# Kernel tuning notes

Hardware: AMD Instinct MI355X
Metric: run time of the kernel (lower is better)

## Reference

```python
import jax, jax.numpy as jnp
import numpy as np

N_X = 32640   # total xlmr subword tokens (64 seqs x 510 tokens)
N_S = 16320   # total stanza word tokens (2 subwords per word)
E = 65280     # dependency edges (bidirectional, avg degree ~4)
D = 768
GCN_DIM = 256
GCN_NUM = 2
POS_DIM = 4
N_UPOS = 17
N_LABEL = 5


def setup_inputs() -> dict:
    key = jax.random.key(0)
    ks = jax.random.split(key, 8)
    x = jax.random.normal(ks[0], (N_X, D), dtype=jnp.float32)
    # mapStanza2Xlmr as segment ids: xlmr token j belongs to stanza word j//2
    seg = jnp.arange(N_X, dtype=jnp.int32) // 2
    edge_index = jax.random.randint(ks[1], (2, E), 0, N_S, dtype=jnp.int32)
    upos_ids = jax.random.randint(ks[2], (N_S,), 0, N_UPOS, dtype=jnp.int32)
    Wc = jax.random.normal(ks[3], (D, GCN_DIM), dtype=jnp.float32) * 0.02
    bc = jnp.zeros((GCN_DIM,), dtype=jnp.float32)
    gcn_W = jax.random.normal(ks[4], (GCN_NUM, GCN_DIM, GCN_DIM), dtype=jnp.float32) * 0.05
    gcn_b = jnp.zeros((GCN_NUM, GCN_DIM), dtype=jnp.float32)
    upos_table = jax.random.normal(ks[5], (N_UPOS, POS_DIM), dtype=jnp.float32)
    Wcls = jax.random.normal(ks[6], (D + GCN_DIM + POS_DIM, N_LABEL), dtype=jnp.float32) * 0.02
    bcls = jnp.zeros((N_LABEL,), dtype=jnp.float32)
    return {"x": x, "seg": seg, "edge_index": edge_index, "upos_ids": upos_ids,
            "Wc": Wc, "bc": bc, "gcn_W": gcn_W, "gcn_b": gcn_b,
            "upos_table": upos_table, "Wcls": Wcls, "bcls": bcls}


def _gcn_conv(h, srcs, dsts, W, b, n):
    # PyG GCNConv: h' = D^-1/2 (A+I) D^-1/2 (h W) + b  (self loops already in srcs/dsts)
    h = h @ W
    deg = jax.ops.segment_sum(jnp.ones_like(dsts, h.dtype), dsts, num_segments=n)
    dinv = jax.lax.rsqrt(deg)  # deg >= 1 because of self loops
    coef = dinv[srcs] * dinv[dsts]
    out = jax.ops.segment_sum(h[srcs] * coef[:, None], dsts, num_segments=n)
    return out + b


def reference(x, seg, edge_index, upos_ids, Wc, bc, gcn_W, gcn_b, upos_table, Wcls, bcls):
    # mapStanza2Xlmr: mean-pool subword embeddings into stanza word embeddings
    cnt = jax.ops.segment_sum(jnp.ones((N_X,), x.dtype), seg, num_segments=N_S)
    stanza = jax.ops.segment_sum(x, seg, num_segments=N_S) / cnt[:, None]  # [N_S, D]
    # GCN over dependency edges (gcn_mode=0: biedges)
    h = stanza @ Wc + bc
    self_idx = jnp.arange(N_S, dtype=edge_index.dtype)
    srcs = jnp.concatenate([edge_index[0], self_idx])
    dsts = jnp.concatenate([edge_index[1], self_idx])
    for i in range(GCN_NUM):
        h = jax.nn.relu(_gcn_conv(h, srcs, dsts, gcn_W[i], gcn_b[i], N_S))
    # POS embedding + concat + relu
    pos = upos_table[upos_ids]                                  # [N_S, POS_DIM]
    info = jax.nn.relu(jnp.concatenate([h, pos], axis=1))       # [N_S, GCN_DIM+POS_DIM]
    # mapXlmr2Stanza: each subword gathers its (single) word's info
    append = info[seg]                                          # [N_X, GCN_DIM+POS_DIM]
    tok = jnp.concatenate([x, append], axis=1)                  # [N_X, 1028]
    logits = jax.nn.relu(tok) @ Wcls + bcls
    return jax.nn.log_softmax(logits, axis=1)
```

## Files before the change

kernel.cpp:

```cpp
#include <hip/hip_runtime.h>

#define NXT 32640
#define NS  16320
#define NE  65280
#define DD  768
#define GD  256
#define NLAB 5
#define CAP 32

typedef __attribute__((ext_vector_type(8))) short bf16x8;
typedef __attribute__((ext_vector_type(8))) unsigned short u16x8;
typedef __attribute__((ext_vector_type(4))) float f32x4;
typedef __attribute__((ext_vector_type(8))) float f32x8;

__device__ inline unsigned short f2b(float f) {
    unsigned int u = __float_as_uint(f);
    unsigned int r = (u + 0x7FFFu + ((u >> 16) & 1u)) >> 16;
    return (unsigned short)r;
}
__device__ inline float b2f(unsigned short h) {
    return __uint_as_float((unsigned int)h << 16);
}

__device__ inline void tile_transpose(const float* __restrict__ src, unsigned short* __restrict__ dst,
                                      int K, int k0, int n0, int tid) {
    __shared__ unsigned short tl[64][65];
#pragma unroll
    for (int i = 0; i < 16; ++i) {
        int idx = tid + i * 256;
        int r = idx >> 6, c = idx & 63;
        tl[r][c] = f2b(src[(size_t)(k0 + r) * GD + n0 + c]);
    }
    __syncthreads();
#pragma unroll
    for (int i = 0; i < 16; ++i) {
        int idx = tid + i * 256;
        int rr = idx >> 6, cc = idx & 63;
        dst[(size_t)(n0 + rr) * K + k0 + cc] = tl[cc][rr];
    }
}

__global__ void k_setup(int* __restrict__ cnt,
                        const float* __restrict__ Wc, unsigned short* __restrict__ WcT,
                        const float* __restrict__ gcn_W, unsigned short* __restrict__ WT,
                        const float* __restrict__ Wcls, float* __restrict__ WclsT,
                        const float* __restrict__ upos_table, const float* __restrict__ bcls,
                        float* __restrict__ posLogit) {
    int b = blockIdx.x, t = threadIdx.x;
    if (b < 64) {
        int i = b * 256 + t;
        if (i < NS) cnt[i] = 0;
    } else if (b < 112) {
        int tile = b - 64;
        tile_transpose(Wc, WcT, DD, (tile >> 2) * 64, (tile & 3) * 64, t);
    } else if (b < 128) {
        int tile = b - 112;
        tile_transpose(gcn_W, WT, GD, (tile >> 2) * 64, (tile & 3) * 64, t);
    } else if (b < 144) {
        int tile = b - 128;
        tile_transpose(gcn_W + (size_t)GD * GD, WT + (size_t)GD * GD, GD,
                       (tile >> 2) * 64, (tile & 3) * 64, t);
    } else if (b < 159) {
        int idx = (b - 144) * 256 + t;
        if (idx < NLAB * DD) {
            int l = idx / DD, k = idx - l * DD;
            WclsT[idx] = Wcls[(size_t)k * NLAB + l];
        }
    } else {
        if (t < 17 * NLAB) {
            int u = t / NLAB, l = t - u * NLAB;
            float a = bcls[l];
#pragma unroll
            for (int p = 0; p < 4; ++p) {
                float pv = upos_table[u * 4 + p];
                pv = pv > 0.f ? pv : 0.f;
                a += pv * Wcls[(size_t)(DD + GD + p) * NLAB + l];
            }
            posLogit[t] = a;
        }
    }
}

__global__ __launch_bounds__(512, 2) void k_mega0(const float* __restrict__ x,
                                                  const unsigned short* __restrict__ WcT,
                                                  const float* __restrict__ WclsT,
                                                  const float* __restrict__ bc,
                                                  const int* __restrict__ ei,
                                                  int* __restrict__ cnt, int* __restrict__ csr_src,
                                                  unsigned short* __restrict__ h_bf,
                                                  float* __restrict__ partial) {
    __shared__ unsigned short lds[2560 * 8];
    const int tid = threadIdx.x;
    if (blockIdx.x >= 255) {
        int e = (blockIdx.x - 255) * 512 + tid;
        if (e < NE) {
            int dst = ei[NE + e];
            int slot = atomicAdd(&cnt[dst], 1);
            if (slot < CAP) csr_src[(size_t)dst * CAP + slot] = ei[e];
        }
        return;
    }
    const int lane = tid & 63;
    const int wv   = tid >> 6;
    const int wr   = wv >> 2, wc = wv & 3;
    const int bm   = blockIdx.x * 64;

    const int kc = tid & 7, rl = (tid >> 3) & 15, g = tid >> 7;
    const int w_loc = g * 16 + rl;
    const float* xr0 = x + (size_t)(2 * (bm + w_loc)) * DD + kc * 8;
    const float* xr1 = xr0 + DD;
    const int aw_slot = (kc >> 2) * 256 + g * 64 + (kc & 3) * 16 + rl;
    const float* wcl = WclsT + kc * 8;

    const unsigned short* srcB[4];
#pragma unroll
    for (int q = 0; q < 4; ++q) {
        int slot = q * 512 + tid;
        int gran = slot >> 8, chunk = slot & 255;
        int nh = gran >> 1, kh = gran & 1;
        int rg = chunk >> 6, kc2 = (chunk >> 4) & 3, rl2 = chunk & 15;
        srcB[q] = WcT + (size_t)(nh * 64 + rg * 16 + rl2) * DD + kh * 32 + kc2 * 8;
    }

    const bf16x8* ldsv = (const bf16x8*)lds;
    f32x4 acc[2][4] = {};
    float lg0[NLAB] = {}, lg1[NLAB] = {};

    for (int it = 0; it < 12; ++it) {
        const int k0 = it * 64;
#pragma unroll
        for (int q = 0; q < 4; ++q)
            __builtin_amdgcn_global_load_lds(srcB[q] + k0, lds + (size_t)(512 + q * 512 + tid) * 8, 16, 0, 0);
        f32x8 va = *(const f32x8*)(xr0 + k0);
        f32x8 vb = *(const f32x8*)(xr1 + k0);
        u16x8 pool;
#pragma unroll
        for (int i = 0; i < 8; ++i) pool[i] = f2b((va[i] + vb[i]) * 0.5f);
        *(u16x8*)(lds + (size_t)aw_slot * 8) = pool;
#pragma unroll
        for (int l = 0; l < NLAB; ++l) {
            f32x8 wv8 = *(const f32x8*)(wcl + (size_t)l * DD + k0);
#pragma unroll
            for (int i = 0; i < 8; ++i) {
                float ra = va[i] > 0.f ? va[i] : 0.f;
                float rb = vb[i] > 0.f ? vb[i] : 0.f;
                lg0[l] += ra * wv8[i];
                lg1[l] += rb * wv8[i];
            }
        }
        __syncthreads();
#pragma unroll
        for (int kh = 0; kh < 2; ++kh) {
            bf16x8 a0 = ldsv[kh * 256 + (wr * 2 + 0) * 64 + lane];
            bf16x8 a1 = ldsv[kh * 256 + (wr * 2 + 1) * 64 + lane];
#pragma unroll
            for (int n = 0; n < 4; ++n) {
                bf16x8 b = ldsv[512 + (wc * 2 + kh) * 256 + n * 64 + lane];
                acc[0][n] = __builtin_amdgcn_mfma_f32_16x16x32_bf16(a0, b, acc[0][n], 0, 0, 0);
                acc[1][n] = __builtin_amdgcn_mfma_f32_16x16x32_bf16(a1, b, acc[1][n], 0, 0, 0);
            }
        }
        __syncthreads();
    }

    const int rl2 = lane & 15, rq = lane >> 4;
#pragma unroll
    for (int m = 0; m < 2; ++m) {
        int row0 = bm + wr * 32 + m * 16 + rq * 4;
#pragma unroll
        for (int n = 0; n < 4; ++n) {
            int col = wc * 64 + n * 16 + rl2;
            float bv = bc[col];
#pragma unroll
            for (int r = 0; r < 4; ++r)
                h_bf[(size_t)(row0 + r) * GD + col] = f2b(acc[m][n][r] + bv);
        }
    }

#pragma unroll
    for (int l = 0; l < NLAB; ++l) {
        lg0[l] += __shfl_xor(lg0[l], 1); lg0[l] += __shfl_xor(lg0[l], 2); lg0[l] += __shfl_xor(lg0[l], 4);
        lg1[l] += __shfl_xor(lg1[l], 1); lg1[l] += __shfl_xor(lg1[l], 2); lg1[l] += __shfl_xor(lg1[l], 4);
    }
    if (kc == 0) {
        int w = bm + w_loc;
        float* pp = partial + (size_t)w * 2 * NLAB;
#pragma unroll
        for (int l = 0; l < NLAB; ++l) { pp[l] = lg0[l]; pp[NLAB + l] = lg1[l]; }
    }
}

__global__ __launch_bounds__(256) void k_gemm(const unsigned short* __restrict__ A,
                                              const unsigned short* __restrict__ BT,
                                              const float* __restrict__ bias,
                                              unsigned short* __restrict__ out,
                                              int K, int nbn) {
    __shared__ unsigned short lds[1536 * 8];
    const int tid  = threadIdx.x;
    const int lane = tid & 63;
    const int wv   = tid >> 6;
    const int wr   = wv >> 1, wc = wv & 1;
    const int bm   = (blockIdx.x / nbn) * 64;
    const int bn   = (blockIdx.x % nbn) * 128;

    const int g  = tid >> 6, w_ = tid & 63, kc = w_ >> 4, rl = w_ & 15;
    const unsigned short* srcA  = A  + (size_t)(bm + g * 16 + rl) * K + kc * 8;
    const unsigned short* srcB0 = BT + (size_t)(bn      + g * 16 + rl) * K + kc * 8;
    const unsigned short* srcB1 = BT + (size_t)(bn + 64 + g * 16 + rl) * K + kc * 8;

    unsigned short* dA0 = lds + (size_t)tid * 8;
    unsigned short* dA1 = dA0 + 256 * 8;
    unsigned short* dB  = lds + (size_t)(512 + tid) * 8;

    const bf16x8* fA = (const bf16x8*)lds + (wr * 2) * 64 + lane;
    const bf16x8* fB = (const bf16x8*)lds + 512 + wc * 256 + lane;

    f32x4 acc[2][4] = {};
    for (int k0 = 0; k0 < K; k0 += 64) {
        __builtin_amdgcn_global_load_lds(srcA  + k0,      dA0,            16, 0, 0);
        __builtin_amdgcn_global_load_lds(srcA  + k0 + 32, dA1,            16, 0, 0);
        __builtin_amdgcn_global_load_lds(srcB0 + k0,      dB,             16, 0, 0);
        __builtin_amdgcn_global_load_lds(srcB1 + k0,      dB + 256 * 8,   16, 0, 0);
        __builtin_amdgcn_global_load_lds(srcB0 + k0 + 32, dB + 512 * 8,   16, 0, 0);
        __builtin_amdgcn_global_load_lds(srcB1 + k0 + 32, dB + 768 * 8,   16, 0, 0);
        __syncthreads();
#pragma unroll
        for (int kh = 0; kh < 2; ++kh) {
            bf16x8 a0 = fA[kh * 256], a1 = fA[kh * 256 + 64];
            const bf16x8* fb = fB + kh * 512;
            bf16x8 b0 = fb[0], b1 = fb[64], b2 = fb[128], b3 = fb[192];
            acc[0][0] = __builtin_amdgcn_mfma_f32_16x16x32_bf16(a0, b0, acc[0][0], 0, 0, 0);
            acc[0][1] = __builtin_amdgcn_mfma_f32_16x16x32_bf16(a0, b1, acc[0][1], 0, 0, 0);
            acc[0][2] = __builtin_amdgcn_mfma_f32_16x16x32_bf16(a0, b2, acc[0][2], 0, 0, 0);
            acc[0][3] = __builtin_amdgcn_mfma_f32_16x16x32_bf16(a0, b3, acc[0][3], 0, 0, 0);
            acc[1][0] = __builtin_amdgcn_mfma_f32_16x16x32_bf16(a1, b0, acc[1][0], 0, 0, 0);
            acc[1][1] = __builtin_amdgcn_mfma_f32_16x16x32_bf16(a1, b1, acc[1][1], 0, 0, 0);
            acc[1][2] = __builtin_amdgcn_mfma_f32_16x16x32_bf16(a1, b2, acc[1][2], 0, 0, 0);
            acc[1][3] = __builtin_amdgcn_mfma_f32_16x16x32_bf16(a1, b3, acc[1][3], 0, 0, 0);
        }
        __syncthreads();
    }

    const int rl2 = lane & 15, rq = lane >> 4;
#pragma unroll
    for (int m = 0; m < 2; ++m) {
        int row0 = bm + wr * 32 + m * 16 + rq * 4;
#pragma unroll
        for (int n = 0; n < 4; ++n) {
            int col = bn + wc * 64 + n * 16 + rl2;
            float bv = bias ? bias[col] : 0.f;
#pragma unroll
            for (int r = 0; r < 4; ++r)
                out[(size_t)(row0 + r) * GD + col] = f2b(acc[m][n][r] + bv);
        }
    }
}

__global__ void k_gather(const int* __restrict__ cnt, const int* __restrict__ csr_src,
                         const unsigned short* __restrict__ hW,
                         const float* __restrict__ b, unsigned short* __restrict__ hout) {
    int w    = blockIdx.x * 4 + (threadIdx.x >> 6);
    int lane = threadIdx.x & 63;
    int c = cnt[w];
    float dw = rsqrtf((float)c + 1.0f);
    const int* sl = csr_src + (size_t)w * CAP;
    float ax = 0.f, ay = 0.f, az = 0.f, aw = 0.f;
    for (int j = 0; j < c; ++j) {
        int src = sl[j];
        float cf = rsqrtf((float)cnt[src] + 1.0f) * dw;
        ushort4 v = *(const ushort4*)&hW[(size_t)src * GD + lane * 4];
        ax += cf * b2f(v.x); ay += cf * b2f(v.y); az += cf * b2f(v.z); aw += cf * b2f(v.w);
    }
    ushort4 sv = *(const ushort4*)&hW[(size_t)w * GD + lane * 4];
    f32x4 bv = *(const f32x4*)&b[lane * 4];
    float c2 = dw * dw;
    float rx = ax + b2f(sv.x) * c2 + bv[0];
    float ry = ay + b2f(sv.y) * c2 + bv[1];
    float rz = az + b2f(sv.z) * c2 + bv[2];
    float rw = aw + b2f(sv.w) * c2 + bv[3];
    ushort4 o;
    o.x = f2b(rx > 0.f ? rx : 0.f);
    o.y = f2b(ry > 0.f ? ry : 0.f);
    o.z = f2b(rz > 0.f ? rz : 0.f);
    o.w = f2b(rw > 0.f ? rw : 0.f);
    *(ushort4*)&hout[(size_t)w * GD + lane * 4] = o;
}

__global__ void k_gather_final(const int* __restrict__ cnt, const int* __restrict__ csr_src,
                               const unsigned short* __restrict__ hW,
                               const float* __restrict__ b,
                               const float* __restrict__ partial,
                               const int* __restrict__ upos_ids,
                               const float* __restrict__ posLogit,
                               const float* __restrict__ Wcls,
                               float* __restrict__ out) {
    int w    = blockIdx.x * 4 + (threadIdx.x >> 6);
    int lane = threadIdx.x & 63;
    int c = cnt[w];
    float dw = rsqrtf((float)c + 1.0f);
    const int* sl = csr_src + (size_t)w * CAP;
    float ax = 0.f, ay = 0.f, az = 0.f, aw = 0.f;
    for (int j = 0; j < c; ++j) {
        int src = sl[j];
        float cf = rsqrtf((float)cnt[src] + 1.0f) * dw;
        ushort4 v = *(const ushort4*)&hW[(size_t)src * GD + lane * 4];
        ax += cf * b2f(v.x); ay += cf * b2f(v.y); az += cf * b2f(v.z); aw += cf * b2f(v.w);
    }
    ushort4 sv = *(const ushort4*)&hW[(size_t)w * GD + lane * 4];
    f32x4 bv = *(const f32x4*)&b[lane * 4];
    float c2 = dw * dw;
    float hv[4];
    hv[0] = ax + b2f(sv.x) * c2 + bv[0];
    hv[1] = ay + b2f(sv.y) * c2 + bv[1];
    hv[2] = az + b2f(sv.z) * c2 + bv[2];
    hv[3] = aw + b2f(sv.w) * c2 + bv[3];
    float acc[NLAB] = {};
#pragma unroll
    for (int i = 0; i < 4; ++i) {
        float v = hv[i] > 0.f ? hv[i] : 0.f;
        const float* wr = Wcls + (size_t)(DD + lane * 4 + i) * NLAB;
#pragma unroll
        for (int l = 0; l < NLAB; ++l) acc[l] += v * wr[l];
    }
#pragma unroll
    for (int off = 32; off > 0; off >>= 1)
#pragma unroll
        for (int l = 0; l < NLAB; ++l) acc[l] += __shfl_xor(acc[l], off);
    if (lane == 0) {
        const float* pl = posLogit + (size_t)upos_ids[w] * NLAB;
        const float* pp = partial + (size_t)w * 2 * NLAB;
#pragma unroll
        for (int t = 0; t < 2; ++t) {
            float lg[NLAB];
#pragma unroll
            for (int l = 0; l < NLAB; ++l) lg[l] = acc[l] + pp[t * NLAB + l] + pl[l];
            float m = lg[0];
#pragma unroll
            for (int l = 1; l < NLAB; ++l) m = fmaxf(m, lg[l]);
            float s = 0.f;
#pragma unroll
            for (int l = 0; l < NLAB; ++l) s += __expf(lg[l] - m);
            float lse = __logf(s) + m;
            float* op = out + (size_t)(2 * w + t) * NLAB;
#pragma unroll
            for (int l = 0; l < NLAB; ++l) op[l] = lg[l] - lse;
        }
    }
}

extern "C" void kernel_launch(void* const* d_in, const int* in_sizes, int n_in,
                              void* d_out, int out_size, void* d_ws, size_t ws_size,
                              hipStream_t stream) {
    const float* x          = (const float*)d_in[0];
    const int*   ei         = (const int*)d_in[2];
    const int*   upos_ids   = (const int*)d_in[3];
    const float* Wc         = (const float*)d_in[4];
    const float* bc         = (const float*)d_in[5];
    const float* gcn_W      = (const float*)d_in[6];
    const float* gcn_b      = (const float*)d_in[7];
    const float* upos_table = (const float*)d_in[8];
    const float* Wcls       = (const float*)d_in[9];
    const float* bcls       = (const float*)d_in[10];
    float* out = (float*)d_out;

    char* ws = (char*)d_ws;
    float* partial          = (float*)ws;            ws += (size_t)NXT * NLAB * 4;
    float* WclsT            = (float*)ws;            ws += (size_t)NLAB * DD * 4;
    float* posLogit         = (float*)ws;            ws += (size_t)17 * NLAB * 4;
    unsigned short* h_bf    = (unsigned short*)ws;   ws += (size_t)NS * GD * 2;
    unsigned short* hW_bf   = (unsigned short*)ws;   ws += (size_t)NS * GD * 2;
    unsigned short* WcT     = (unsigned short*)ws;   ws += (size_t)DD * GD * 2;
    unsigned short* WT      = (unsigned short*)ws;   ws += (size_t)2 * GD * GD * 2;
    int* cnt                = (int*)ws;              ws += (size_t)NS * 4;
    int* csr_src            = (int*)ws;              ws += (size_t)NS * CAP * 4;

    k_setup<<<160, 256, 0, stream>>>(cnt, Wc, WcT, gcn_W, WT, Wcls, WclsT,
                                     upos_table, bcls, posLogit);
    k_mega0<<<510, 512, 0, stream>>>(x, WcT, WclsT, bc, ei, cnt, csr_src, h_bf, partial);
    k_gemm<<<(NS / 64) * 2, 256, 0, stream>>>(h_bf, WT, nullptr, hW_bf, GD, 2);
    k_gather<<<NS / 4, 256, 0, stream>>>(cnt, csr_src, hW_bf, gcn_b, h_bf);
    k_gemm<<<(NS / 64) * 2, 256, 0, stream>>>(h_bf, WT + (size_t)GD * GD, nullptr, hW_bf, GD, 2);
    k_gather_final<<<NS / 4, 256, 0, stream>>>(cnt, csr_src, hW_bf, gcn_b + GD,
                                               partial, upos_ids, posLogit, Wcls, out);
}
```

Measured before the change: 113.2 us.

## Split mega0 GEMM across two N-halves with XCD-aware block mapping

The fused pooling+Wc GEMM kernel now launches two blocks per 64-row tile, each computing 128 of the 256 output columns. This doubles the block count for better occupancy on the 256 CUs and halves LDS per block. Blocks are remapped so consecutive row tiles land on the same XCD. The cost is that each row tile's x loads and pooling are now done twice. Only the bn==0 block computes the classifier partial logits.

```diff
diff --git a/kernel.cpp b/kernel.cpp
--- a/kernel.cpp
+++ b/kernel.cpp
@@ -89,10 +89,10 @@
                                                   int* __restrict__ cnt, int* __restrict__ csr_src,
                                                   unsigned short* __restrict__ h_bf,
                                                   float* __restrict__ partial) {
-    __shared__ unsigned short lds[2560 * 8];
+    __shared__ unsigned short lds[1536 * 8];
     const int tid = threadIdx.x;
-    if (blockIdx.x >= 255) {
-        int e = (blockIdx.x - 255) * 512 + tid;
+    if (blockIdx.x >= 512) {
+        int e = (blockIdx.x - 512) * 512 + tid;
         if (e < NE) {
             int dst = ei[NE + e];
             int slot = atomicAdd(&cnt[dst], 1);
@@ -100,10 +100,15 @@
         }
         return;
     }
+    const int xcd = blockIdx.x & 7, slot = blockIdx.x >> 3;
+    const int bm64 = (slot >> 1) * 8 + xcd;
+    const int bn   = slot & 1;
+    if (bm64 >= 255) return;
+    const int bm = bm64 * 64;
+
     const int lane = tid & 63;
     const int wv   = tid >> 6;
-    const int wr   = wv >> 2, wc = wv & 3;
-    const int bm   = blockIdx.x * 64;
+    const int wr   = wv & 3, wc = wv >> 2;
 
     const int kc = tid & 7, rl = (tid >> 3) & 15, g = tid >> 7;
     const int w_loc = g * 16 + rl;
@@ -112,24 +117,24 @@
     const int aw_slot = (kc >> 2) * 256 + g * 64 + (kc & 3) * 16 + rl;
     const float* wcl = WclsT + kc * 8;
 
-    const unsigned short* srcB[4];
-#pragma unroll
-    for (int q = 0; q < 4; ++q) {
-        int slot = q * 512 + tid;
-        int gran = slot >> 8, chunk = slot & 255;
+    const unsigned short* srcB[2];
+#pragma unroll
+    for (int q = 0; q < 2; ++q) {
+        int s = q * 512 + tid;
+        int gran = s >> 8, chunk = s & 255;
         int nh = gran >> 1, kh = gran & 1;
         int rg = chunk >> 6, kc2 = (chunk >> 4) & 3, rl2 = chunk & 15;
-        srcB[q] = WcT + (size_t)(nh * 64 + rg * 16 + rl2) * DD + kh * 32 + kc2 * 8;
+        srcB[q] = WcT + (size_t)(bn * 128 + nh * 64 + rg * 16 + rl2) * DD + kh * 32 + kc2 * 8;
     }
 
     const bf16x8* ldsv = (const bf16x8*)lds;
-    f32x4 acc[2][4] = {};
+    f32x4 acc[4] = {};
     float lg0[NLAB] = {}, lg1[NLAB] = {};
 
     for (int it = 0; it < 12; ++it) {
         const int k0 = it * 64;
 #pragma unroll
-        for (int q = 0; q < 4; ++q)
+        for (int q = 0; q < 2; ++q)
             __builtin_amdgcn_global_load_lds(srcB[q] + k0, lds + (size_t)(512 + q * 512 + tid) * 8, 16, 0, 0);
         f32x8 va = *(const f32x8*)(xr0 + k0);
         f32x8 vb = *(const f32x8*)(xr1 + k0);
@@ -137,56 +142,57 @@
 #pragma unroll
         for (int i = 0; i < 8; ++i) pool[i] = f2b((va[i] + vb[i]) * 0.5f);
         *(u16x8*)(lds + (size_t)aw_slot * 8) = pool;
-#pragma unroll
-        for (int l = 0; l < NLAB; ++l) {
-            f32x8 wv8 = *(const f32x8*)(wcl + (size_t)l * DD + k0);
-#pragma unroll
-            for (int i = 0; i < 8; ++i) {
-                float ra = va[i] > 0.f ? va[i] : 0.f;
-                float rb = vb[i] > 0.f ? vb[i] : 0.f;
-                lg0[l] += ra * wv8[i];
-                lg1[l] += rb * wv8[i];
+        if (bn == 0) {
+#pragma unroll
+            for (int l = 0; l < NLAB; ++l) {
+                f32x8 wv8 = *(const f32x8*)(wcl + (size_t)l * DD + k0);
+#pragma unroll
+                for (int i = 0; i < 8; ++i) {
+                    float ra = va[i] > 0.f ? va[i] : 0.f;
+                    float rb = vb[i] > 0.f ? vb[i] : 0.f;
+                    lg0[l] += ra * wv8[i];
+                    lg1[l] += rb * wv8[i];
+                }
             }
         }
         __syncthreads();
 #pragma unroll
         for (int kh = 0; kh < 2; ++kh) {
-            bf16x8 a0 = ldsv[kh * 256 + (wr * 2 + 0) * 64 + lane];
-            bf16x8 a1 = ldsv[kh * 256 + (wr * 2 + 1) * 64 + lane];
+            bf16x8 a = ldsv[kh * 256 + wr * 64 + lane];
 #pragma unroll
             for (int n = 0; n < 4; ++n) {
                 bf16x8 b = ldsv[512 + (wc * 2 + kh) * 256 + n * 64 + lane];
-                acc[0][n] = __builtin_amdgcn_mfma_f32_16x16x32_bf16(a0, b, acc[0][n], 0, 0, 0);
-                acc[1][n] = __builtin_amdgcn_mfma_f32_16x16x32_bf16(a1, b, acc[1][n], 0, 0, 0);
+                acc[n] = __builtin_amdgcn_mfma_f32_16x16x32_bf16(a, b, acc[n], 0, 0, 0);
             }
         }
         __syncthreads();
     }
 
     const int rl2 = lane & 15, rq = lane >> 4;
-#pragma unroll
-    for (int m = 0; m < 2; ++m) {
-        int row0 = bm + wr * 32 + m * 16 + rq * 4;
+    {
+        int row0 = bm + wr * 16 + rq * 4;
 #pragma unroll
         for (int n = 0; n < 4; ++n) {
-            int col = wc * 64 + n * 16 + rl2;
+            int col = bn * 128 + wc * 64 + n * 16 + rl2;
             float bv = bc[col];
 #pragma unroll
             for (int r = 0; r < 4; ++r)
-                h_bf[(size_t)(row0 + r) * GD + col] = f2b(acc[m][n][r] + bv);
-        }
-    }
-
-#pragma unroll
-    for (int l = 0; l < NLAB; ++l) {
-        lg0[l] += __shfl_xor(lg0[l], 1); lg0[l] += __shfl_xor(lg0[l], 2); lg0[l] += __shfl_xor(lg0[l], 4);
-        lg1[l] += __shfl_xor(lg1[l], 1); lg1[l] += __shfl_xor(lg1[l], 2); lg1[l] += __shfl_xor(lg1[l], 4);
-    }
-    if (kc == 0) {
-        int w = bm + w_loc;
-        float* pp = partial + (size_t)w * 2 * NLAB;
-#pragma unroll
-        for (int l = 0; l < NLAB; ++l) { pp[l] = lg0[l]; pp[NLAB + l] = lg1[l]; }
+                h_bf[(size_t)(row0 + r) * GD + col] = f2b(acc[n][r] + bv);
+        }
+    }
+
+    if (bn == 0) {
+#pragma unroll
+        for (int l = 0; l < NLAB; ++l) {
+            lg0[l] += __shfl_xor(lg0[l], 1); lg0[l] += __shfl_xor(lg0[l], 2); lg0[l] += __shfl_xor(lg0[l], 4);
+            lg1[l] += __shfl_xor(lg1[l], 1); lg1[l] += __shfl_xor(lg1[l], 2); lg1[l] += __shfl_xor(lg1[l], 4);
+        }
+        if (kc == 0) {
+            int w = bm + w_loc;
+            float* pp = partial + (size_t)w * 2 * NLAB;
+#pragma unroll
+            for (int l = 0; l < NLAB; ++l) { pp[l] = lg0[l]; pp[NLAB + l] = lg1[l]; }
+        }
     }
 }
 
@@ -376,7 +382,7 @@
 
     k_setup<<<160, 256, 0, stream>>>(cnt, Wc, WcT, gcn_W, WT, Wcls, WclsT,
                                      upos_table, bcls, posLogit);
-    k_mega0<<<510, 512, 0, stream>>>(x, WcT, WclsT, bc, ei, cnt, csr_src, h_bf, partial);
+    k_mega0<<<640, 512, 0, stream>>>(x, WcT, WclsT, bc, ei, cnt, csr_src, h_bf, partial);
     k_gemm<<<(NS / 64) * 2, 256, 0, stream>>>(h_bf, WT, nullptr, hW_bf, GD, 2);
     k_gather<<<NS / 4, 256, 0, stream>>>(cnt, csr_src, hW_bf, gcn_b, h_bf);
     k_gemm<<<(NS / 64) * 2, 256, 0, stream>>>(h_bf, WT + (size_t)GD * GD, nullptr, hW_bf, GD, 2);
```

Result: no change. 115.0 us (+1.5%).

## Load MFMA operands directly from global into registers, dropping LDS staging

Applied to the files above, without the earlier changes.

The fused pooling, projection and logit kernel no longer stages pooled activations and WcT tiles in shared memory. Each wave now loads its A rows from x and its B columns from WcT straight into MFMA register layout, so both __syncthreads per K step go away. Only the wc==0 waves compute the classifier partial logits, and the launch shrinks to exactly the number of blocks the GEMM and edge-CSR work need. The cost is that the four column waves each read the same x rows, raising cache traffic, and the logit FMAs are concentrated in a quarter of the waves.

```diff
diff --git a/kernel.cpp b/kernel.cpp
--- a/kernel.cpp
+++ b/kernel.cpp
@@ -9,7 +9,6 @@
 #define CAP 32
 
 typedef __attribute__((ext_vector_type(8))) short bf16x8;
-typedef __attribute__((ext_vector_type(8))) unsigned short u16x8;
 typedef __attribute__((ext_vector_type(4))) float f32x4;
 typedef __attribute__((ext_vector_type(8))) float f32x8;
 
@@ -81,15 +80,14 @@
     }
 }
 
-__global__ __launch_bounds__(512, 2) void k_mega0(const float* __restrict__ x,
-                                                  const unsigned short* __restrict__ WcT,
-                                                  const float* __restrict__ WclsT,
-                                                  const float* __restrict__ bc,
-                                                  const int* __restrict__ ei,
-                                                  int* __restrict__ cnt, int* __restrict__ csr_src,
-                                                  unsigned short* __restrict__ h_bf,
-                                                  float* __restrict__ partial) {
-    __shared__ unsigned short lds[2560 * 8];
+__global__ __launch_bounds__(512) void k_mega0(const float* __restrict__ x,
+                                               const unsigned short* __restrict__ WcT,
+                                               const float* __restrict__ WclsT,
+                                               const float* __restrict__ bc,
+                                               const int* __restrict__ ei,
+                                               int* __restrict__ cnt, int* __restrict__ csr_src,
+                                               unsigned short* __restrict__ h_bf,
+                                               float* __restrict__ partial) {
     const int tid = threadIdx.x;
     if (blockIdx.x >= 255) {
         int e = (blockIdx.x - 255) * 512 + tid;
@@ -100,67 +98,65 @@
         }
         return;
     }
+    const int bm   = blockIdx.x * 64;
     const int lane = tid & 63;
     const int wv   = tid >> 6;
-    const int wr   = wv >> 2, wc = wv & 3;
-    const int bm   = blockIdx.x * 64;
-
-    const int kc = tid & 7, rl = (tid >> 3) & 15, g = tid >> 7;
-    const int w_loc = g * 16 + rl;
-    const float* xr0 = x + (size_t)(2 * (bm + w_loc)) * DD + kc * 8;
-    const float* xr1 = xr0 + DD;
-    const int aw_slot = (kc >> 2) * 256 + g * 64 + (kc & 3) * 16 + rl;
-    const float* wcl = WclsT + kc * 8;
-
-    const unsigned short* srcB[4];
-#pragma unroll
-    for (int q = 0; q < 4; ++q) {
-        int slot = q * 512 + tid;
-        int gran = slot >> 8, chunk = slot & 255;
-        int nh = gran >> 1, kh = gran & 1;
-        int rg = chunk >> 6, kc2 = (chunk >> 4) & 3, rl2 = chunk & 15;
-        srcB[q] = WcT + (size_t)(nh * 64 + rg * 16 + rl2) * DD + kh * 32 + kc2 * 8;
-    }
-
-    const bf16x8* ldsv = (const bf16x8*)lds;
+    const int wr   = wv >> 2;
+    const int wc   = wv & 3;
+    const int rl   = lane & 15;
+    const int kg   = (lane >> 4) * 8;
+    const bool do_lg = (wc == 0);
+
+    const float* xr0[2];
+#pragma unroll
+    for (int m = 0; m < 2; ++m)
+        xr0[m] = x + (size_t)(2 * (bm + wr * 32 + m * 16 + rl)) * DD + kg;
+
+    const unsigned short* bcol[4];
+#pragma unroll
+    for (int n = 0; n < 4; ++n)
+        bcol[n] = WcT + (size_t)(wc * 64 + n * 16 + rl) * DD + kg;
+
+    const float* wcl = WclsT + kg;
+
     f32x4 acc[2][4] = {};
-    float lg0[NLAB] = {}, lg1[NLAB] = {};
-
+    float lg[2][2][NLAB] = {};
+
+#pragma unroll 2
     for (int it = 0; it < 12; ++it) {
         const int k0 = it * 64;
-#pragma unroll
-        for (int q = 0; q < 4; ++q)
-            __builtin_amdgcn_global_load_lds(srcB[q] + k0, lds + (size_t)(512 + q * 512 + tid) * 8, 16, 0, 0);
-        f32x8 va = *(const f32x8*)(xr0 + k0);
-        f32x8 vb = *(const f32x8*)(xr1 + k0);
-        u16x8 pool;
-#pragma unroll
-        for (int i = 0; i < 8; ++i) pool[i] = f2b((va[i] + vb[i]) * 0.5f);
-        *(u16x8*)(lds + (size_t)aw_slot * 8) = pool;
-#pragma unroll
-        for (int l = 0; l < NLAB; ++l) {
-            f32x8 wv8 = *(const f32x8*)(wcl + (size_t)l * DD + k0);
-#pragma unroll
-            for (int i = 0; i < 8; ++i) {
-                float ra = va[i] > 0.f ? va[i] : 0.f;
-                float rb = vb[i] > 0.f ? vb[i] : 0.f;
-                lg0[l] += ra * wv8[i];
-                lg1[l] += rb * wv8[i];
+        bf16x8 a[2][2];
+#pragma unroll
+        for (int m = 0; m < 2; ++m)
+#pragma unroll
+            for (int kh = 0; kh < 2; ++kh) {
+                f32x8 va = *(const f32x8*)(xr0[m] + k0 + kh * 32);
+                f32x8 vb = *(const f32x8*)(xr0[m] + DD + k0 + kh * 32);
+#pragma unroll
+                for (int i = 0; i < 8; ++i)
+                    a[m][kh][i] = (short)f2b((va[i] + vb[i]) * 0.5f);
+                if (do_lg) {
+#pragma unroll
+                    for (int l = 0; l < NLAB; ++l) {
+                        f32x8 w8 = *(const f32x8*)(wcl + (size_t)l * DD + k0 + kh * 32);
+#pragma unroll
+                        for (int i = 0; i < 8; ++i) {
+                            float ra = va[i] > 0.f ? va[i] : 0.f;
+                            float rb = vb[i] > 0.f ? vb[i] : 0.f;
+                            lg[m][0][l] += ra * w8[i];
+                            lg[m][1][l] += rb * w8[i];
+                        }
+                    }
+                }
             }
-        }
-        __syncthreads();
-#pragma unroll
-        for (int kh = 0; kh < 2; ++kh) {
-            bf16x8 a0 = ldsv[kh * 256 + (wr * 2 + 0) * 64 + lane];
-            bf16x8 a1 = ldsv[kh * 256 + (wr * 2 + 1) * 64 + lane];
+#pragma unroll
+        for (int kh = 0; kh < 2; ++kh)
 #pragma unroll
             for (int n = 0; n < 4; ++n) {
-                bf16x8 b = ldsv[512 + (wc * 2 + kh) * 256 + n * 64 + lane];
-                acc[0][n] = __builtin_amdgcn_mfma_f32_16x16x32_bf16(a0, b, acc[0][n], 0, 0, 0);
-                acc[1][n] = __builtin_amdgcn_mfma_f32_16x16x32_bf16(a1, b, acc[1][n], 0, 0, 0);
+                bf16x8 b = *(const bf16x8*)(bcol[n] + k0 + kh * 32);
+                acc[0][n] = __builtin_amdgcn_mfma_f32_16x16x32_bf16(a[0][kh], b, acc[0][n], 0, 0, 0);
+                acc[1][n] = __builtin_amdgcn_mfma_f32_16x16x32_bf16(a[1][kh], b, acc[1][n], 0, 0, 0);
             }
-        }
-        __syncthreads();
     }
 
     const int rl2 = lane & 15, rq = lane >> 4;
@@ -177,16 +173,28 @@
         }
     }
 
-#pragma unroll
-    for (int l = 0; l < NLAB; ++l) {
-        lg0[l] += __shfl_xor(lg0[l], 1); lg0[l] += __shfl_xor(lg0[l], 2); lg0[l] += __shfl_xor(lg0[l], 4);
-        lg1[l] += __shfl_xor(lg1[l], 1); lg1[l] += __shfl_xor(lg1[l], 2); lg1[l] += __shfl_xor(lg1[l], 4);
-    }
-    if (kc == 0) {
-        int w = bm + w_loc;
-        float* pp = partial + (size_t)w * 2 * NLAB;
-#pragma unroll
-        for (int l = 0; l < NLAB; ++l) { pp[l] = lg0[l]; pp[NLAB + l] = lg1[l]; }
+    if (do_lg) {
+#pragma unroll
+        for (int m = 0; m < 2; ++m)
+#pragma unroll
+            for (int p = 0; p < 2; ++p)
+#pragma unroll
+                for (int l = 0; l < NLAB; ++l) {
+                    lg[m][p][l] += __shfl_xor(lg[m][p][l], 16);
+                    lg[m][p][l] += __shfl_xor(lg[m][p][l], 32);
+                }
+        if (lane < 16) {
+#pragma unroll
+            for (int m = 0; m < 2; ++m) {
+                int w = bm + wr * 32 + m * 16 + rl;
+                float* pp = partial + (size_t)w * 2 * NLAB;
+#pragma unroll
+                for (int l = 0; l < NLAB; ++l) {
+                    pp[l]        = lg[m][0][l];
+                    pp[NLAB + l] = lg[m][1][l];
+                }
+            }
+        }
     }
 }
 
@@ -376,7 +384,7 @@
 
     k_setup<<<160, 256, 0, stream>>>(cnt, Wc, WcT, gcn_W, WT, Wcls, WclsT,
                                      upos_table, bcls, posLogit);
-    k_mega0<<<510, 512, 0, stream>>>(x, WcT, WclsT, bc, ei, cnt, csr_src, h_bf, partial);
+    k_mega0<<<383, 512, 0, stream>>>(x, WcT, WclsT, bc, ei, cnt, csr_src, h_bf, partial);
     k_gemm<<<(NS / 64) * 2, 256, 0, stream>>>(h_bf, WT, nullptr, hW_bf, GD, 2);
     k_gather<<<NS / 4, 256, 0, stream>>>(cnt, csr_src, hW_bf, gcn_b, h_bf);
     k_gemm<<<(NS / 64) * 2, 256, 0, stream>>>(h_bf, WT + (size_t)GD * GD, nullptr, hW_bf, GD, 2);
```

New measurement: 160.9 us. +42.1%, slower.
